# Kernel tuning notes

Measured on AMD Instinct MI355X. Metric: run time of the kernel, lower is better.

The kernel has to match this reference:

```python
import jax, jax.numpy as jnp
import numpy as np

B, T, H, A = 64, 512, 1024, 300


def setup_inputs() -> dict:
    key = jax.random.key(0)
    ks = jax.random.split(key, 12)
    s = 0.02  # weight init scale
    return {
        "hidden": jax.random.normal(ks[0], (B, T, H), jnp.float32),
        "aspect": jax.random.normal(ks[1], (B, 1, A), jnp.float32),
        # torch Linear stores weight as [out_features, in_features]
        "W_h": jax.random.normal(ks[2], (H, H), jnp.float32) * s,
        "b_h": jax.random.normal(ks[3], (H,), jnp.float32) * s,
        "W_v": jax.random.normal(ks[4], (A, A), jnp.float32) * s,
        "b_v": jax.random.normal(ks[5], (A,), jnp.float32) * s,
        "w_w": jax.random.normal(ks[6], (1, H + A), jnp.float32) * s,
        "w_b": jax.random.normal(ks[7], (1,), jnp.float32) * s,
        "W_p": jax.random.normal(ks[8], (H, H), jnp.float32) * s,
        "b_p": jax.random.normal(ks[9], (H,), jnp.float32) * s,
        "W_x": jax.random.normal(ks[10], (H, H), jnp.float32) * s,
        "b_x": jax.random.normal(ks[11], (H,), jnp.float32) * s,
    }


def reference(hidden, aspect, W_h, b_h, W_v, b_v, w_w, w_b, W_p, b_p, W_x, b_x):
    # transformed aspect: [B, 1, A], repeated along seq dim -> [B, T, A]
    tv = aspect @ W_v.T + b_v
    rep_v = jnp.broadcast_to(tv, (hidden.shape[0], hidden.shape[1], tv.shape[-1]))
    # M = tanh(concat(W_h(hidden), repeated_v)) : [B, T, H+A]
    M = jnp.tanh(jnp.concatenate([hidden @ W_h.T + b_h, rep_v], axis=-1))
    # additive attention scores -> softmax over T
    scores = jnp.einsum("bts,os->bto", M, w_w)[..., 0] + w_b[0]  # [B, T]
    alpha = jax.nn.softmax(scores, axis=-1)
    # weighted sum r = alpha^T @ hidden : [B, 1, H]
    r = jnp.einsum("bt,bth->bh", alpha, hidden)[:, None, :]
    # NOTE: faithful to original torch broadcasting quirk:
    # [B,1,H] + [B,H] broadcasts to [B,B,H]
    output = jnp.tanh((r @ W_p.T + b_p) + (hidden[:, -1, :] @ W_x.T + b_x))
    return output
```

## Files before the change

kernel.cpp:

```cpp
#include <hip/hip_runtime.h>
#include <hip/hip_bf16.h>
#include <stdint.h>

#define B_DIM 64
#define T_DIM 512
#define H_DIM 1024
#define M_DIM (B_DIM * T_DIM)

typedef __bf16 bf16x8 __attribute__((ext_vector_type(8)));
typedef float f32x4 __attribute__((ext_vector_type(4)));

__device__ __forceinline__ float tanh_fast(float x) {
  float e = __expf(2.0f * x);
  return 1.0f - 2.0f / (e + 1.0f);
}

__device__ __forceinline__ void async_cp16(const void* gp, void* lp) {
  __builtin_amdgcn_global_load_lds(
      reinterpret_cast<const __attribute__((address_space(1))) uint32_t*>(
          reinterpret_cast<uintptr_t>(gp)),
      reinterpret_cast<__attribute__((address_space(3))) uint32_t*>(
          reinterpret_cast<uintptr_t>(lp)),
      16, 0, 0);
}

__global__ void cvt_kernel(const float* __restrict__ src, __bf16* __restrict__ dst, int n4) {
  int i = blockIdx.x * 256 + threadIdx.x;
  if (i >= n4) return;
  float4 v = reinterpret_cast<const float4*>(src)[i];
  union { __bf16 b[4]; uint2 u; } o;
  o.b[0] = (__bf16)v.x; o.b[1] = (__bf16)v.y; o.b[2] = (__bf16)v.z; o.b[3] = (__bf16)v.w;
  reinterpret_cast<uint2*>(dst)[i] = o.u;
}

#define GM_BK 64
__global__ __launch_bounds__(256) void gemm_scores_kernel(
    const __bf16* __restrict__ A, const __bf16* __restrict__ Bm,
    const float* __restrict__ bh, const float* __restrict__ ww,
    float* __restrict__ scores, int K) {
  __shared__ __attribute__((aligned(16))) __bf16 lA[128 * GM_BK];
  __shared__ __attribute__((aligned(16))) __bf16 lB[128 * GM_BK];

  const int tid = threadIdx.x;
  const int m0 = blockIdx.y * 128;
  const int n0 = blockIdx.x * 128;

  const int wv = tid >> 6;
  const int lane = tid & 63;
  const int wm = wv & 1, wn = wv >> 1;
  const int r16 = lane & 15, quad = lane >> 4;

  f32x4 acc[4][4] = {};

  const __bf16* gA[4]; const __bf16* gB[4];
  __bf16* lAd[4]; __bf16* lBd[4];
#pragma unroll
  for (int j = 0; j < 4; ++j) {
    int c = j * 256 + tid;
    int row = c >> 3;
    int p = c & 7;
    int kc = p ^ ((row >> 1) & 7);
    gA[j] = A + (size_t)(m0 + row) * K + kc * 8;
    gB[j] = Bm + (size_t)(n0 + row) * K + kc * 8;
    lAd[j] = &lA[c * 8];
    lBd[j] = &lB[c * 8];
  }

  const int sw = r16 >> 1;
  const __bf16* pa[2]; const __bf16* pb[2];
#pragma unroll
  for (int kk = 0; kk < 2; ++kk) {
    pa[kk] = &lA[(wm * 64 + r16) * GM_BK + ((kk * 4 + quad) ^ sw) * 8];
    pb[kk] = &lB[(wn * 64 + r16) * GM_BK + ((kk * 4 + quad) ^ sw) * 8];
  }

  for (int k0 = 0; k0 < K; k0 += GM_BK) {
#pragma unroll
    for (int j = 0; j < 4; ++j) async_cp16(gA[j] + k0, lAd[j]);
#pragma unroll
    for (int j = 0; j < 4; ++j) async_cp16(gB[j] + k0, lBd[j]);
    __syncthreads();
#pragma unroll
    for (int kk = 0; kk < 2; ++kk) {
      bf16x8 af[4], bfr[4];
#pragma unroll
      for (int i = 0; i < 4; ++i) af[i] = *reinterpret_cast<const bf16x8*>(pa[kk] + i * 16 * GM_BK);
#pragma unroll
      for (int i = 0; i < 4; ++i) bfr[i] = *reinterpret_cast<const bf16x8*>(pb[kk] + i * 16 * GM_BK);
#pragma unroll
      for (int mi = 0; mi < 4; ++mi)
#pragma unroll
        for (int ni = 0; ni < 4; ++ni)
          acc[mi][ni] = __builtin_amdgcn_mfma_f32_16x16x32_bf16(af[mi], bfr[ni], acc[mi][ni], 0, 0, 0);
    }
    __syncthreads();
  }

  float bhv[4], wwv[4];
#pragma unroll
  for (int ni = 0; ni < 4; ++ni) {
    int n = n0 + wn * 64 + ni * 16 + r16;
    bhv[ni] = bh[n];
    wwv[ni] = ww[n];
  }
#pragma unroll
  for (int mi = 0; mi < 4; ++mi) {
#pragma unroll
    for (int rg = 0; rg < 4; ++rg) {
      float s = 0.f;
#pragma unroll
      for (int ni = 0; ni < 4; ++ni)
        s += tanh_fast(acc[mi][ni][rg] + bhv[ni]) * wwv[ni];
      s += __shfl_xor(s, 1, 16);
      s += __shfl_xor(s, 2, 16);
      s += __shfl_xor(s, 4, 16);
      s += __shfl_xor(s, 8, 16);
      if (r16 == 0) {
        int m = m0 + wm * 64 + mi * 16 + quad * 4 + rg;
        atomicAdd(&scores[m], s);
      }
    }
  }
}

__global__ void softmax_kernel(const float* __restrict__ scores, float* __restrict__ alpha) {
  __shared__ float wred[4], wsum[4];
  const int b = blockIdx.x, tid = threadIdx.x;
  const int wv = tid >> 6, lane = tid & 63;
  float v0 = scores[b * T_DIM + tid];
  float v1 = scores[b * T_DIM + 256 + tid];
  float mx = fmaxf(v0, v1);
#pragma unroll
  for (int off = 1; off < 64; off <<= 1) mx = fmaxf(mx, __shfl_xor(mx, off, 64));
  if (lane == 0) wred[wv] = mx;
  __syncthreads();
  mx = fmaxf(fmaxf(wred[0], wred[1]), fmaxf(wred[2], wred[3]));
  float e0 = __expf(v0 - mx), e1 = __expf(v1 - mx);
  float s = e0 + e1;
#pragma unroll
  for (int off = 1; off < 64; off <<= 1) s += __shfl_xor(s, off, 64);
  if (lane == 0) wsum[wv] = s;
  __syncthreads();
  s = wsum[0] + wsum[1] + wsum[2] + wsum[3];
  float inv = 1.0f / s;
  alpha[b * T_DIM + tid] = e0 * inv;
  alpha[b * T_DIM + 256 + tid] = e1 * inv;
}

__global__ void weighted_sum_kernel(const float* __restrict__ hidden,
                                    const float* __restrict__ alpha,
                                    float* __restrict__ r) {
  __shared__ float al[64];
  const int b = blockIdx.y, tc = blockIdx.x, tid = threadIdx.x;
  if (tid < 64) al[tid] = alpha[b * T_DIM + tc * 64 + tid];
  __syncthreads();
  const float* hp = hidden + (size_t)b * T_DIM * H_DIM + (size_t)tc * 64 * H_DIM + tid * 4;
  float4 acc = make_float4(0.f, 0.f, 0.f, 0.f);
#pragma unroll 8
  for (int t = 0; t < 64; ++t) {
    float a = al[t];
    float4 v = *reinterpret_cast<const float4*>(hp + (size_t)t * H_DIM);
    acc.x += a * v.x; acc.y += a * v.y; acc.z += a * v.z; acc.w += a * v.w;
  }
  float* rp = r + b * H_DIM + tid * 4;
  atomicAdd(rp + 0, acc.x);
  atomicAdd(rp + 1, acc.y);
  atomicAdd(rp + 2, acc.z);
  atomicAdd(rp + 3, acc.w);
}

__global__ void rowvec_matT_kernel(const float* __restrict__ src, size_t src_stride,
                                   const float* __restrict__ W, const float* __restrict__ bias,
                                   float* __restrict__ dst) {
  __shared__ float sv[H_DIM];
  const int i = blockIdx.y, h0 = blockIdx.x * 64, tid = threadIdx.x;
  reinterpret_cast<float4*>(sv)[tid] =
      reinterpret_cast<const float4*>(src + (size_t)i * src_stride)[tid];
  __syncthreads();
  const int hl = tid >> 2;
  const int kq = tid & 3;
  const float* wr = W + (size_t)(h0 + hl) * H_DIM + kq * 256;
  const float* svp = sv + kq * 256;
  float acc = 0.f;
#pragma unroll 4
  for (int k = 0; k < 256; k += 4) {
    float4 w4 = *reinterpret_cast<const float4*>(wr + k);
    float4 s4 = *reinterpret_cast<const float4*>(svp + k);
    acc += w4.x * s4.x + w4.y * s4.y + w4.z * s4.z + w4.w * s4.w;
  }
  acc += __shfl_xor(acc, 1, 4);
  acc += __shfl_xor(acc, 2, 4);
  if (kq == 0) dst[(size_t)i * H_DIM + h0 + hl] = acc + bias[h0 + hl];
}

__global__ void final_kernel(const float* __restrict__ rp, const float* __restrict__ xq,
                             float* __restrict__ out) {
  int idx = blockIdx.x * 256 + threadIdx.x;
  int e = idx * 4;
  int i = e >> 16;
  int j = (e >> 10) & 63;
  int h = e & 1023;
  float4 a = *reinterpret_cast<const float4*>(&rp[i * H_DIM + h]);
  float4 b = *reinterpret_cast<const float4*>(&xq[j * H_DIM + h]);
  float4 o;
  o.x = tanh_fast(a.x + b.x);
  o.y = tanh_fast(a.y + b.y);
  o.z = tanh_fast(a.z + b.z);
  o.w = tanh_fast(a.w + b.w);
  *reinterpret_cast<float4*>(&out[e]) = o;
}

extern "C" void kernel_launch(void* const* d_in, const int* in_sizes, int n_in,
                              void* d_out, int out_size, void* d_ws, size_t ws_size,
                              hipStream_t stream) {
  const float* hidden = (const float*)d_in[0];
  const float* W_h = (const float*)d_in[2];
  const float* b_h = (const float*)d_in[3];
  const float* w_w = (const float*)d_in[6];
  const float* W_p = (const float*)d_in[8];
  const float* b_p = (const float*)d_in[9];
  const float* W_x = (const float*)d_in[10];
  const float* b_x = (const float*)d_in[11];
  float* out = (float*)d_out;

  char* ws = (char*)d_ws;
  __bf16* hidBf = (__bf16*)ws;
  __bf16* whBf = (__bf16*)(ws + 67108864);
  float* scores = (float*)(ws + 69206016);
  float* alpha = (float*)(ws + 69337088);
  float* r = (float*)(ws + 69468160);
  float* rp = (float*)(ws + 69730304);
  float* xq = (float*)(ws + 69992448);

  cvt_kernel<<<(M_DIM * H_DIM / 4) / 256, 256, 0, stream>>>(hidden, hidBf, M_DIM * H_DIM / 4);
  cvt_kernel<<<(H_DIM * H_DIM / 4) / 256, 256, 0, stream>>>(W_h, whBf, H_DIM * H_DIM / 4);

  hipMemsetAsync(scores, 0, M_DIM * sizeof(float), stream);
  hipMemsetAsync(r, 0, B_DIM * H_DIM * sizeof(float), stream);
  gemm_scores_kernel<<<dim3(H_DIM / 128, M_DIM / 128), 256, 0, stream>>>(
      hidBf, whBf, b_h, w_w, scores, H_DIM);

  softmax_kernel<<<B_DIM, 256, 0, stream>>>(scores, alpha);

  weighted_sum_kernel<<<dim3(8, B_DIM), 256, 0, stream>>>(hidden, alpha, r);

  rowvec_matT_kernel<<<dim3(H_DIM / 64, B_DIM), 256, 0, stream>>>(r, (size_t)H_DIM, W_p, b_p, rp);
  rowvec_matT_kernel<<<dim3(H_DIM / 64, B_DIM), 256, 0, stream>>>(
      hidden + (size_t)(T_DIM - 1) * H_DIM, (size_t)T_DIM * H_DIM, W_x, b_x, xq);

  final_kernel<<<(B_DIM * B_DIM * H_DIM / 4) / 256, 256, 0, stream>>>(rp, xq, out);
}
```

Measured before the change: 424.1 us.

## Merge prep, softmax, weighted-sum and projection kernels; load GEMM B operand directly to registers

Combines the two bf16 conversions and the two memsets into one prep kernel, folds softmax into the weighted-sum blocks, and runs the W_x projection as extra blocks of that same launch. The rp projection now uses one block per batch row that loops over all outputs. The GEMM drops the LDS tile for W_h and loads B fragments straight from global memory into registers. Block order is remapped so consecutive blocks share the same W_h column tile. This cuts launch count and LDS traffic, at the cost of redundant softmax work per block, uncached-by-LDS B loads, and fewer, longer blocks for the projections.

Result: slower. 687.7 us (+62.2%).

```diff
diff --git a/kernel.cpp b/kernel.cpp
--- a/kernel.cpp
+++ b/kernel.cpp
@@ -24,13 +24,29 @@
       16, 0, 0);
 }
 
-__global__ void cvt_kernel(const float* __restrict__ src, __bf16* __restrict__ dst, int n4) {
-  int i = blockIdx.x * 256 + threadIdx.x;
-  if (i >= n4) return;
-  float4 v = reinterpret_cast<const float4*>(src)[i];
-  union { __bf16 b[4]; uint2 u; } o;
-  o.b[0] = (__bf16)v.x; o.b[1] = (__bf16)v.y; o.b[2] = (__bf16)v.z; o.b[3] = (__bf16)v.w;
-  reinterpret_cast<uint2*>(dst)[i] = o.u;
+__global__ void prep_kernel(const float* __restrict__ hid, const float* __restrict__ Wh,
+                            __bf16* __restrict__ hidBf, __bf16* __restrict__ whBf,
+                            float* __restrict__ scores, float* __restrict__ r) {
+  int bid = blockIdx.x, tid = threadIdx.x;
+  if (bid < 32768) {
+    int i = bid * 256 + tid;
+    float4 v = reinterpret_cast<const float4*>(hid)[i];
+    union { __bf16 b[4]; uint2 u; } o;
+    o.b[0] = (__bf16)v.x; o.b[1] = (__bf16)v.y; o.b[2] = (__bf16)v.z; o.b[3] = (__bf16)v.w;
+    reinterpret_cast<uint2*>(hidBf)[i] = o.u;
+  } else if (bid < 33792) {
+    int i = (bid - 32768) * 256 + tid;
+    float4 v = reinterpret_cast<const float4*>(Wh)[i];
+    union { __bf16 b[4]; uint2 u; } o;
+    o.b[0] = (__bf16)v.x; o.b[1] = (__bf16)v.y; o.b[2] = (__bf16)v.z; o.b[3] = (__bf16)v.w;
+    reinterpret_cast<uint2*>(whBf)[i] = o.u;
+  } else if (bid < 33824) {
+    int i = (bid - 33792) * 256 + tid;
+    reinterpret_cast<float4*>(scores)[i] = make_float4(0.f, 0.f, 0.f, 0.f);
+  } else {
+    int i = (bid - 33824) * 256 + tid;
+    reinterpret_cast<float4*>(r)[i] = make_float4(0.f, 0.f, 0.f, 0.f);
+  }
 }
 
 #define GM_BK 64
@@ -39,11 +55,11 @@
     const float* __restrict__ bh, const float* __restrict__ ww,
     float* __restrict__ scores, int K) {
   __shared__ __attribute__((aligned(16))) __bf16 lA[128 * GM_BK];
-  __shared__ __attribute__((aligned(16))) __bf16 lB[128 * GM_BK];
 
   const int tid = threadIdx.x;
-  const int m0 = blockIdx.y * 128;
-  const int n0 = blockIdx.x * 128;
+  const int bid = blockIdx.x;
+  const int m0 = (bid & 255) * 128;
+  const int n0 = (bid >> 8) * 128;
 
   const int wv = tid >> 6;
   const int lane = tid & 63;
@@ -52,8 +68,8 @@
 
   f32x4 acc[4][4] = {};
 
-  const __bf16* gA[4]; const __bf16* gB[4];
-  __bf16* lAd[4]; __bf16* lBd[4];
+  const __bf16* gA[4];
+  __bf16* lAd[4];
 #pragma unroll
   for (int j = 0; j < 4; ++j) {
     int c = j * 256 + tid;
@@ -61,37 +77,38 @@
     int p = c & 7;
     int kc = p ^ ((row >> 1) & 7);
     gA[j] = A + (size_t)(m0 + row) * K + kc * 8;
-    gB[j] = Bm + (size_t)(n0 + row) * K + kc * 8;
     lAd[j] = &lA[c * 8];
-    lBd[j] = &lB[c * 8];
   }
 
   const int sw = r16 >> 1;
-  const __bf16* pa[2]; const __bf16* pb[2];
-#pragma unroll
-  for (int kk = 0; kk < 2; ++kk) {
+  const __bf16* pa[2];
+#pragma unroll
+  for (int kk = 0; kk < 2; ++kk)
     pa[kk] = &lA[(wm * 64 + r16) * GM_BK + ((kk * 4 + quad) ^ sw) * 8];
-    pb[kk] = &lB[(wn * 64 + r16) * GM_BK + ((kk * 4 + quad) ^ sw) * 8];
-  }
+
+  const __bf16* gBfr = Bm + (size_t)(n0 + wn * 64 + r16) * K + quad * 8;
 
   for (int k0 = 0; k0 < K; k0 += GM_BK) {
 #pragma unroll
     for (int j = 0; j < 4; ++j) async_cp16(gA[j] + k0, lAd[j]);
-#pragma unroll
-    for (int j = 0; j < 4; ++j) async_cp16(gB[j] + k0, lBd[j]);
+    bf16x8 bAll[2][4];
+#pragma unroll
+    for (int kk = 0; kk < 2; ++kk)
+#pragma unroll
+      for (int ni = 0; ni < 4; ++ni)
+        bAll[kk][ni] = *reinterpret_cast<const bf16x8*>(
+            gBfr + (size_t)ni * 16 * K + k0 + kk * 32);
     __syncthreads();
 #pragma unroll
     for (int kk = 0; kk < 2; ++kk) {
-      bf16x8 af[4], bfr[4];
+      bf16x8 af[4];
 #pragma unroll
       for (int i = 0; i < 4; ++i) af[i] = *reinterpret_cast<const bf16x8*>(pa[kk] + i * 16 * GM_BK);
 #pragma unroll
-      for (int i = 0; i < 4; ++i) bfr[i] = *reinterpret_cast<const bf16x8*>(pb[kk] + i * 16 * GM_BK);
-#pragma unroll
       for (int mi = 0; mi < 4; ++mi)
 #pragma unroll
         for (int ni = 0; ni < 4; ++ni)
-          acc[mi][ni] = __builtin_amdgcn_mfma_f32_16x16x32_bf16(af[mi], bfr[ni], acc[mi][ni], 0, 0, 0);
+          acc[mi][ni] = __builtin_amdgcn_mfma_f32_16x16x32_bf16(af[mi], bAll[kk][ni], acc[mi][ni], 0, 0, 0);
     }
     __syncthreads();
   }
@@ -123,74 +140,95 @@
   }
 }
 
-__global__ void softmax_kernel(const float* __restrict__ scores, float* __restrict__ alpha) {
-  __shared__ float wred[4], wsum[4];
-  const int b = blockIdx.x, tid = threadIdx.x;
-  const int wv = tid >> 6, lane = tid & 63;
-  float v0 = scores[b * T_DIM + tid];
-  float v1 = scores[b * T_DIM + 256 + tid];
-  float mx = fmaxf(v0, v1);
-#pragma unroll
-  for (int off = 1; off < 64; off <<= 1) mx = fmaxf(mx, __shfl_xor(mx, off, 64));
-  if (lane == 0) wred[wv] = mx;
+__global__ void wsum_xq_kernel(const float* __restrict__ scores,
+                               const float* __restrict__ hidden,
+                               const float* __restrict__ Wx, const float* __restrict__ bx,
+                               float* __restrict__ r, float* __restrict__ xq) {
+  __shared__ float sv[H_DIM];
+  __shared__ float red[8];
+  const int bid = blockIdx.x, tid = threadIdx.x;
+  if (bid < 512) {
+    const int b = bid >> 3, tc = bid & 7;
+    const int wv = tid >> 6, lane = tid & 63;
+    float v0 = scores[b * T_DIM + tid];
+    float v1 = scores[b * T_DIM + 256 + tid];
+    float mx = fmaxf(v0, v1);
+#pragma unroll
+    for (int off = 1; off < 64; off <<= 1) mx = fmaxf(mx, __shfl_xor(mx, off, 64));
+    if (lane == 0) red[wv] = mx;
+    __syncthreads();
+    mx = fmaxf(fmaxf(red[0], red[1]), fmaxf(red[2], red[3]));
+    float e0 = __expf(v0 - mx), e1 = __expf(v1 - mx);
+    float s = e0 + e1;
+#pragma unroll
+    for (int off = 1; off < 64; off <<= 1) s += __shfl_xor(s, off, 64);
+    if (lane == 0) red[4 + wv] = s;
+    __syncthreads();
+    float inv = 1.0f / (red[4] + red[5] + red[6] + red[7]);
+    if (tid < 64) sv[tid] = __expf(scores[b * T_DIM + tc * 64 + tid] - mx) * inv;
+    __syncthreads();
+    const float* hp = hidden + (size_t)b * T_DIM * H_DIM + (size_t)tc * 64 * H_DIM + tid * 4;
+    float4 acc = make_float4(0.f, 0.f, 0.f, 0.f);
+#pragma unroll 8
+    for (int t = 0; t < 64; ++t) {
+      float a = sv[t];
+      float4 v = *reinterpret_cast<const float4*>(hp + (size_t)t * H_DIM);
+      acc.x += a * v.x; acc.y += a * v.y; acc.z += a * v.z; acc.w += a * v.w;
+    }
+    float* rp = r + b * H_DIM + tid * 4;
+    atomicAdd(rp + 0, acc.x);
+    atomicAdd(rp + 1, acc.y);
+    atomicAdd(rp + 2, acc.z);
+    atomicAdd(rp + 3, acc.w);
+  } else {
+    const int i = bid - 512;
+    reinterpret_cast<float4*>(sv)[tid] = reinterpret_cast<const float4*>(
+        hidden + (size_t)i * T_DIM * H_DIM + (size_t)(T_DIM - 1) * H_DIM)[tid];
+    __syncthreads();
+    const int hl = tid >> 2, kq = tid & 3;
+    const float* svp = sv + kq * 256;
+#pragma unroll 2
+    for (int hc = 0; hc < 16; ++hc) {
+      int h = hc * 64 + hl;
+      const float* wr = Wx + (size_t)h * H_DIM + kq * 256;
+      float acc = 0.f;
+#pragma unroll 4
+      for (int k = 0; k < 256; k += 4) {
+        float4 w4 = *reinterpret_cast<const float4*>(wr + k);
+        float4 s4 = *reinterpret_cast<const float4*>(svp + k);
+        acc += w4.x * s4.x + w4.y * s4.y + w4.z * s4.z + w4.w * s4.w;
+      }
+      acc += __shfl_xor(acc, 1, 4);
+      acc += __shfl_xor(acc, 2, 4);
+      if (kq == 0) xq[(size_t)i * H_DIM + h] = acc + bx[h];
+    }
+  }
+}
+
+__global__ void rp_kernel(const float* __restrict__ r, const float* __restrict__ Wp,
+                          const float* __restrict__ bp, float* __restrict__ rp) {
+  __shared__ float sv[H_DIM];
+  const int i = blockIdx.x, tid = threadIdx.x;
+  reinterpret_cast<float4*>(sv)[tid] =
+      reinterpret_cast<const float4*>(r + (size_t)i * H_DIM)[tid];
   __syncthreads();
-  mx = fmaxf(fmaxf(wred[0], wred[1]), fmaxf(wred[2], wred[3]));
-  float e0 = __expf(v0 - mx), e1 = __expf(v1 - mx);
-  float s = e0 + e1;
-#pragma unroll
-  for (int off = 1; off < 64; off <<= 1) s += __shfl_xor(s, off, 64);
-  if (lane == 0) wsum[wv] = s;
-  __syncthreads();
-  s = wsum[0] + wsum[1] + wsum[2] + wsum[3];
-  float inv = 1.0f / s;
-  alpha[b * T_DIM + tid] = e0 * inv;
-  alpha[b * T_DIM + 256 + tid] = e1 * inv;
-}
-
-__global__ void weighted_sum_kernel(const float* __restrict__ hidden,
-                                    const float* __restrict__ alpha,
-                                    float* __restrict__ r) {
-  __shared__ float al[64];
-  const int b = blockIdx.y, tc = blockIdx.x, tid = threadIdx.x;
-  if (tid < 64) al[tid] = alpha[b * T_DIM + tc * 64 + tid];
-  __syncthreads();
-  const float* hp = hidden + (size_t)b * T_DIM * H_DIM + (size_t)tc * 64 * H_DIM + tid * 4;
-  float4 acc = make_float4(0.f, 0.f, 0.f, 0.f);
-#pragma unroll 8
-  for (int t = 0; t < 64; ++t) {
-    float a = al[t];
-    float4 v = *reinterpret_cast<const float4*>(hp + (size_t)t * H_DIM);
-    acc.x += a * v.x; acc.y += a * v.y; acc.z += a * v.z; acc.w += a * v.w;
-  }
-  float* rp = r + b * H_DIM + tid * 4;
-  atomicAdd(rp + 0, acc.x);
-  atomicAdd(rp + 1, acc.y);
-  atomicAdd(rp + 2, acc.z);
-  atomicAdd(rp + 3, acc.w);
-}
-
-__global__ void rowvec_matT_kernel(const float* __restrict__ src, size_t src_stride,
-                                   const float* __restrict__ W, const float* __restrict__ bias,
-                                   float* __restrict__ dst) {
-  __shared__ float sv[H_DIM];
-  const int i = blockIdx.y, h0 = blockIdx.x * 64, tid = threadIdx.x;
-  reinterpret_cast<float4*>(sv)[tid] =
-      reinterpret_cast<const float4*>(src + (size_t)i * src_stride)[tid];
-  __syncthreads();
-  const int hl = tid >> 2;
-  const int kq = tid & 3;
-  const float* wr = W + (size_t)(h0 + hl) * H_DIM + kq * 256;
+  const int hl = tid >> 2, kq = tid & 3;
   const float* svp = sv + kq * 256;
-  float acc = 0.f;
+#pragma unroll 2
+  for (int hc = 0; hc < 16; ++hc) {
+    int h = hc * 64 + hl;
+    const float* wr = Wp + (size_t)h * H_DIM + kq * 256;
+    float acc = 0.f;
 #pragma unroll 4
-  for (int k = 0; k < 256; k += 4) {
-    float4 w4 = *reinterpret_cast<const float4*>(wr + k);
-    float4 s4 = *reinterpret_cast<const float4*>(svp + k);
-    acc += w4.x * s4.x + w4.y * s4.y + w4.z * s4.z + w4.w * s4.w;
-  }
-  acc += __shfl_xor(acc, 1, 4);
-  acc += __shfl_xor(acc, 2, 4);
-  if (kq == 0) dst[(size_t)i * H_DIM + h0 + hl] = acc + bias[h0 + hl];
+    for (int k = 0; k < 256; k += 4) {
+      float4 w4 = *reinterpret_cast<const float4*>(wr + k);
+      float4 s4 = *reinterpret_cast<const float4*>(svp + k);
+      acc += w4.x * s4.x + w4.y * s4.y + w4.z * s4.z + w4.w * s4.w;
+    }
+    acc += __shfl_xor(acc, 1, 4);
+    acc += __shfl_xor(acc, 2, 4);
+    if (kq == 0) rp[(size_t)i * H_DIM + h] = acc + bp[h];
+  }
 }
 
 __global__ void final_kernel(const float* __restrict__ rp, const float* __restrict__ xq,
@@ -227,26 +265,17 @@
   __bf16* hidBf = (__bf16*)ws;
   __bf16* whBf = (__bf16*)(ws + 67108864);
   float* scores = (float*)(ws + 69206016);
-  float* alpha = (float*)(ws + 69337088);
   float* r = (float*)(ws + 69468160);
   float* rp = (float*)(ws + 69730304);
   float* xq = (float*)(ws + 69992448);
 
-  cvt_kernel<<<(M_DIM * H_DIM / 4) / 256, 256, 0, stream>>>(hidden, hidBf, M_DIM * H_DIM / 4);
-  cvt_kernel<<<(H_DIM * H_DIM / 4) / 256, 256, 0, stream>>>(W_h, whBf, H_DIM * H_DIM / 4);
-
-  hipMemsetAsync(scores, 0, M_DIM * sizeof(float), stream);
-  hipMemsetAsync(r, 0, B_DIM * H_DIM * sizeof(float), stream);
-  gemm_scores_kernel<<<dim3(H_DIM / 128, M_DIM / 128), 256, 0, stream>>>(
-      hidBf, whBf, b_h, w_w, scores, H_DIM);
-
-  softmax_kernel<<<B_DIM, 256, 0, stream>>>(scores, alpha);
-
-  weighted_sum_kernel<<<dim3(8, B_DIM), 256, 0, stream>>>(hidden, alpha, r);
-
-  rowvec_matT_kernel<<<dim3(H_DIM / 64, B_DIM), 256, 0, stream>>>(r, (size_t)H_DIM, W_p, b_p, rp);
-  rowvec_matT_kernel<<<dim3(H_DIM / 64, B_DIM), 256, 0, stream>>>(
-      hidden + (size_t)(T_DIM - 1) * H_DIM, (size_t)T_DIM * H_DIM, W_x, b_x, xq);
+  prep_kernel<<<33888, 256, 0, stream>>>(hidden, W_h, hidBf, whBf, scores, r);
+
+  gemm_scores_kernel<<<2048, 256, 0, stream>>>(hidBf, whBf, b_h, w_w, scores, H_DIM);
+
+  wsum_xq_kernel<<<576, 256, 0, stream>>>(scores, hidden, W_x, b_x, r, xq);
+
+  rp_kernel<<<B_DIM, 256, 0, stream>>>(r, W_p, b_p, rp);
 
   final_kernel<<<(B_DIM * B_DIM * H_DIM / 4) / 256, 256, 0, stream>>>(rp, xq, out);
 }
```
